# Kernel tuning notes

Measured on AMD Instinct MI355X. Metric: run time of the kernel, lower is better.

## Reference

```python
import jax, jax.numpy as jnp
import numpy as np

B, H, S, D = 2, 12, 2048, 64

def setup_inputs() -> dict:
    key = jax.random.key(0)
    kq, kk, kv = jax.random.split(key, 3)
    q = jax.random.normal(kq, (B, H, S, D), dtype=jnp.float32)
    k = jax.random.normal(kk, (B, H, S, D), dtype=jnp.float32)
    v = jax.random.normal(kv, (B, H, S, D), dtype=jnp.float32)
    attn_mask = jnp.zeros((1, 1, S, S), dtype=jnp.float32)
    return {"q": q, "k": k, "v": v, "attn_mask": attn_mask}

def reference(q, k, v, attn_mask):
    # scores: [B, H, S, S]
    scale = 1.0 / jnp.sqrt(jnp.asarray(q.shape[-1], q.dtype))
    attn = jnp.einsum('bhqd,bhkd->bhqk', q, k) * scale
    attn = attn + attn_mask  # additive mask, broadcast over batch/heads
    attn = jax.nn.softmax(attn, axis=-1)
    # dropout_ratio == 0.0 -> dropout is identity
    out = jnp.einsum('bhqk,bhkd->bhqd', attn, v)
    return out
```

## Files before the change

kernel.cpp:

```cpp
#include <hip/hip_runtime.h>
#include <hip/hip_bf16.h>
#include <stdint.h>

#define SLEN  2048
#define DHEAD 64
#define LOG2E 1.4426950408889634f
#define QSCALE (0.125f * LOG2E)

typedef short bf16x8 __attribute__((ext_vector_type(8)));
typedef float f32x4  __attribute__((ext_vector_type(4)));
typedef float f32x16 __attribute__((ext_vector_type(16)));
typedef unsigned short u16x8 __attribute__((ext_vector_type(8)));
typedef unsigned u32x2 __attribute__((ext_vector_type(2)));

static __device__ __forceinline__ unsigned short f2bf(float f) {
    union { float f; unsigned int u; } x; x.f = f;
    return (unsigned short)((x.u + 0x7FFFu + ((x.u >> 16) & 1u)) >> 16);
}

static __device__ __forceinline__ unsigned pk2(float lo, float hi) {
    __hip_bfloat162 h = __float22bfloat162_rn(make_float2(lo, hi));
    union { __hip_bfloat162 b; unsigned u; } c; c.b = h; return c.u;
}

static __device__ __forceinline__ u32x2 pl32(unsigned a, unsigned b) {
    return __builtin_amdgcn_permlane32_swap(a, b, false, false);
}
static __device__ __forceinline__ float    asf(unsigned u) { union { unsigned u; float f; } c; c.u = u; return c.f; }
static __device__ __forceinline__ unsigned asu(float f)    { union { float f; unsigned u; } c; c.f = f; return c.u; }
static __device__ __forceinline__ float max3(float a, float b, float c) {
    return fmaxf(fmaxf(a, b), c);
}

static __device__ __forceinline__ void gl_lds16(const void* g, void* l) {
    __builtin_amdgcn_global_load_lds(
        (const __attribute__((address_space(1))) unsigned int*)g,
        (__attribute__((address_space(3))) unsigned int*)l, 16, 0, 0);
}

__global__ __launch_bounds__(256)
void prep(const float* __restrict__ K, const float* __restrict__ V,
          const float* __restrict__ Mk, unsigned* __restrict__ flag, int maskN4,
          unsigned short* __restrict__ Kb, unsigned short* __restrict__ Vt)
{
    __shared__ unsigned short T[64][72];
    const int tid = threadIdx.x;
    const int st = blockIdx.x, bh = blockIdx.y;
    const size_t base = ((size_t)bh * SLEN + (size_t)st * 64) * DHEAD;

    #pragma unroll
    for (int it = 0; it < 4; ++it) {
        const int idx = it * 1024 + tid * 4;
        const int s = idx >> 6, d = idx & 63;
        float4 k4 = *(const float4*)(K + base + idx);
        float4 v4 = *(const float4*)(V + base + idx);
        ushort4 ko;
        ko.x = f2bf(k4.x); ko.y = f2bf(k4.y);
        ko.z = f2bf(k4.z); ko.w = f2bf(k4.w);
        *(ushort4*)(Kb + base + idx) = ko;
        T[d + 0][s] = f2bf(v4.x);
        T[d + 1][s] = f2bf(v4.y);
        T[d + 2][s] = f2bf(v4.z);
        T[d + 3][s] = f2bf(v4.w);
    }
    __syncthreads();
    const int d = tid >> 2, sc = (tid & 3) * 16;
    unsigned short* orow = Vt + ((size_t)bh * DHEAD + d) * SLEN + (size_t)st * 64 + sc;
    *(u16x8*)(orow)     = *(const u16x8*)&T[d][sc];
    *(u16x8*)(orow + 8) = *(const u16x8*)&T[d][sc + 8];

    const int nb  = gridDim.x * gridDim.y;
    const int bid = blockIdx.y * gridDim.x + blockIdx.x;
    unsigned any = 0;
    for (int i = bid * 256 + tid; i < maskN4; i += nb * 256) {
        float4 mv = *(const float4*)(Mk + (size_t)i * 4);
        any |= asu(mv.x) | asu(mv.y) | asu(mv.z) | asu(mv.w);
    }
    if (any) atomicOr(flag, 1u);
}

__global__ __launch_bounds__(256, 3)
void sdpa_fwd11(const float* __restrict__ Q,
                const unsigned short* __restrict__ Kb,
                const unsigned short* __restrict__ VtG,
                const float* __restrict__ M, const unsigned* __restrict__ flag,
                float* __restrict__ O,
                float* __restrict__ Opart, float* __restrict__ ML,
                int nsShift, int BH)
{
    __shared__ unsigned short Kt[2][64][64];
    __shared__ unsigned short Vt[2][64][64];

    const int tid  = threadIdx.x;
    const int wave = tid >> 6, lane = tid & 63;
    const int l31  = lane & 31, hi = lane >> 5;
    const bool hasMask = (*flag != 0);

    const int nwg  = gridDim.x;
    int wg = blockIdx.x;
    if ((nwg & 7) == 0) wg = (wg & 7) * (nwg >> 3) + (wg >> 3);
    const int qt    = wg & 15;
    const int rest  = wg >> 4;
    const int slice = rest & ((1 << nsShift) - 1);
    const int bh    = rest >> nsShift;

    const int kv0 = slice * (SLEN >> nsShift);
    const int NT  = (SLEN >> nsShift) >> 6;
    const int qrow = qt * 128 + wave * 32 + l31;
    const size_t hoff = (size_t)bh * SLEN * DHEAD;

    bf16x8 qf[4];
    {
        const float* qp = Q + hoff + (size_t)qrow * DHEAD + hi * 8;
        #pragma unroll
        for (int ds = 0; ds < 4; ++ds) {
            float4 a = *(const float4*)(qp + ds * 16);
            float4 b = *(const float4*)(qp + ds * 16 + 4);
            union { unsigned u[4]; bf16x8 v; } fq;
            fq.u[0] = pk2(a.x * QSCALE, a.y * QSCALE);
            fq.u[1] = pk2(a.z * QSCALE, a.w * QSCALE);
            fq.u[2] = pk2(b.x * QSCALE, b.y * QSCALE);
            fq.u[3] = pk2(b.z * QSCALE, b.w * QSCALE);
            qf[ds] = fq.v;
        }
    }

    const char* kgb = (const char*)(Kb + hoff) + (size_t)kv0 * 128;
    const char* vgb = (const char*)(VtG + (size_t)bh * DHEAD * SLEN) + (size_t)kv0 * 2;
    unsigned koff[2], voff[2], ldst[2];
    #pragma unroll
    for (int i = 0; i < 2; ++i) {
        const unsigned o = i * 4096 + tid * 16;
        const unsigned row = o >> 7;
        const unsigned slot = ((o >> 4) & 7) ^ (row & 7) ^ ((row >> 3) & 7);
        koff[i] = row * 128 + slot * 16;
        voff[i] = row * 4096 + slot * 16;
        ldst[i] = i * 4096 + wave * 1024;
    }

    f32x16 oacc[2];
    #pragma unroll
    for (int db = 0; db < 2; ++db)
        #pragma unroll
        for (int r = 0; r < 16; ++r) oacc[db][r] = 0.f;
    float m_i = -INFINITY, l_i = 0.f;

    auto STAGE = [&](int tt) {
        const unsigned bo = (unsigned)(tt & 1) * 8192;
        #pragma unroll
        for (int i = 0; i < 2; ++i) {
            gl_lds16(kgb + (size_t)tt * 8192 + koff[i], (char*)Kt + bo + ldst[i]);
            gl_lds16(vgb + (size_t)tt * 128  + voff[i], (char*)Vt + bo + ldst[i]);
        }
    };

    STAGE(0);

    for (int kt = 0; kt < NT; ++kt) {
        const int b0 = kt & 1;

        asm volatile("s_waitcnt vmcnt(0)" ::: "memory");
        __builtin_amdgcn_s_barrier();
        __builtin_amdgcn_sched_barrier(0);

        if (kt + 1 < NT) STAGE(kt + 1);

        float4 mq[8];
        if (hasMask) {
            const float* mrow = M + (size_t)qrow * SLEN + kv0 + kt * 64;
            #pragma unroll
            for (int sb = 0; sb < 2; ++sb)
                #pragma unroll
                for (int g = 0; g < 4; ++g)
                    mq[sb * 4 + g] = *(const float4*)(mrow + sb * 32 + g * 8 + hi * 4);
        }

        f32x16 sc[2];
        const char* kl = (const char*)Kt + b0 * 8192;
        __builtin_amdgcn_s_setprio(1);
        #pragma unroll
        for (int sb = 0; sb < 2; ++sb) {
            f32x16 acc;
            #pragma unroll
            for (int r = 0; r < 16; ++r) acc[r] = 0.f;
            const int row = sb * 32 + l31;
            const int rx = (row & 7) ^ ((row >> 3) & 7);
            #pragma unroll
            for (int ds = 0; ds < 4; ++ds) {
                const int slot = (ds * 2 + hi) ^ rx;
                bf16x8 kf = *(const bf16x8*)(kl + row * 128 + slot * 16);
                acc = __builtin_amdgcn_mfma_f32_32x32x16_bf16(kf, qf[ds], acc, 0, 0, 0);
            }
            sc[sb] = acc;
        }
        __builtin_amdgcn_s_setprio(0);

        if (hasMask) {
            #pragma unroll
            for (int sb = 0; sb < 2; ++sb)
                #pragma unroll
                for (int r = 0; r < 16; ++r)
                    sc[sb][r] = fmaf(mq[sb * 4 + (r >> 2)][r & 3], LOG2E, sc[sb][r]);
        }

        float red[8];
        #pragma unroll
        for (int r = 0; r < 8; ++r)
            red[r] = fmaxf(fmaxf(sc[0][r], sc[0][r + 8]),
                           fmaxf(sc[1][r], sc[1][r + 8]));
        float r0 = max3(red[0], red[1], red[2]);
        float r1 = max3(red[3], red[4], red[5]);
        float r2 = max3(fmaxf(red[6], red[7]), r0, r1);
        u32x2 pm = pl32(asu(r2), asu(r2));
        const float mtile = fmaxf(asf(pm.x), asf(pm.y));

        if (!__all(mtile - m_i <= 11.0f)) {
            const float mnew = fmaxf(m_i, mtile);
            const float alpha = __builtin_amdgcn_exp2f(m_i - mnew);
            l_i *= alpha;
            #pragma unroll
            for (int db = 0; db < 2; ++db)
                #pragma unroll
                for (int r = 0; r < 16; ++r) oacc[db][r] *= alpha;
            m_i = mnew;
        }

        #pragma unroll
        for (int sb = 0; sb < 2; ++sb)
            #pragma unroll
            for (int r = 0; r < 16; ++r)
                sc[sb][r] = __builtin_amdgcn_exp2f(sc[sb][r] - m_i);

        float sr[16];
        #pragma unroll
        for (int r = 0; r < 16; ++r) sr[r] = sc[0][r] + sc[1][r];
        #pragma unroll
        for (int r = 0; r < 8; ++r) sr[r] += sr[r + 8];
        #pragma unroll
        for (int r = 0; r < 4; ++r) sr[r] += sr[r + 4];
        sr[0] = (sr[0] + sr[2]) + (sr[1] + sr[3]);
        u32x2 ps = pl32(asu(sr[0]), asu(sr[0]));
        l_i += asf(ps.x) + asf(ps.y);

        unsigned wa[8], wb[8];
        #pragma unroll
        for (int sb = 0; sb < 2; ++sb)
            #pragma unroll
            for (int g = 0; g < 4; ++g) {
                wa[sb * 4 + g] = pk2(sc[sb][4 * g + 0], sc[sb][4 * g + 1]);
                wb[sb * 4 + g] = pk2(sc[sb][4 * g + 2], sc[sb][4 * g + 3]);
            }
        bf16x8 pf[4];
        #pragma unroll
        for (int ks = 0; ks < 4; ++ks) {
            u32x2 pa = pl32(wa[2 * ks], wa[2 * ks + 1]);
            u32x2 pb = pl32(wb[2 * ks], wb[2 * ks + 1]);
            union { unsigned u[4]; bf16x8 v; } f;
            f.u[0] = pa.x;
            f.u[1] = pb.x;
            f.u[2] = pa.y;
            f.u[3] = pb.y;
            pf[ks] = f.v;
        }

        const char* vl = (const char*)Vt + b0 * 8192;
        __builtin_amdgcn_s_setprio(1);
        #pragma unroll
        for (int db = 0; db < 2; ++db) {
            const int row = db * 32 + l31;
            const int rx = (row & 7) ^ ((row >> 3) & 7);
            #pragma unroll
            for (int ks = 0; ks < 4; ++ks) {
                const int slot = (ks * 2 + hi) ^ rx;
                bf16x8 vf = *(const bf16x8*)(vl + row * 128 + slot * 16);
                oacc[db] = __builtin_amdgcn_mfma_f32_32x32x16_bf16(vf, pf[ks], oacc[db], 0, 0, 0);
            }
        }
        __builtin_amdgcn_s_setprio(0);
    }

    if (nsShift == 0) {
        const float inv = 1.0f / l_i;
        float* op = O + hoff + (size_t)qrow * DHEAD;
        #pragma unroll
        for (int db = 0; db < 2; ++db)
            #pragma unroll
            for (int g = 0; g < 4; ++g) {
                float4 o4;
                o4.x = oacc[db][4 * g + 0] * inv;
                o4.y = oacc[db][4 * g + 1] * inv;
                o4.z = oacc[db][4 * g + 2] * inv;
                o4.w = oacc[db][4 * g + 3] * inv;
                *(float4*)(op + db * 32 + g * 8 + hi * 4) = o4;
            }
    } else {
        const size_t pidx = ((size_t)slice * BH + bh) * SLEN + qrow;
        float* op = Opart + pidx * DHEAD;
        #pragma unroll
        for (int db = 0; db < 2; ++db)
            #pragma unroll
            for (int g = 0; g < 4; ++g) {
                float4 o4;
                o4.x = oacc[db][4 * g + 0];
                o4.y = oacc[db][4 * g + 1];
                o4.z = oacc[db][4 * g + 2];
                o4.w = oacc[db][4 * g + 3];
                *(float4*)(op + db * 32 + g * 8 + hi * 4) = o4;
            }
        if (hi == 0) {
            ML[pidx * 2]     = m_i;
            ML[pidx * 2 + 1] = l_i;
        }
    }
}

__global__ __launch_bounds__(256)
void merge_partials(const float* __restrict__ Opart, const float* __restrict__ ML,
                    float* __restrict__ O, int NS, int BHS)
{
    const int gid = blockIdx.x * 256 + threadIdx.x;
    const int row = gid >> 4;
    const int c = (gid & 15) << 2;
    if (row >= BHS) return;

    float m = -INFINITY;
    for (int s = 0; s < NS; ++s)
        m = fmaxf(m, ML[((size_t)s * BHS + row) * 2]);

    float lsum = 0.f;
    float4 acc = make_float4(0.f, 0.f, 0.f, 0.f);
    for (int s = 0; s < NS; ++s) {
        const size_t pr = (size_t)s * BHS + row;
        const float w = __builtin_amdgcn_exp2f(ML[pr * 2] - m);
        lsum += w * ML[pr * 2 + 1];
        float4 v = *(const float4*)(Opart + pr * DHEAD + c);
        acc.x += w * v.x; acc.y += w * v.y;
        acc.z += w * v.z; acc.w += w * v.w;
    }
    const float inv = 1.0f / lsum;
    float4 o4;
    o4.x = acc.x * inv; o4.y = acc.y * inv;
    o4.z = acc.z * inv; o4.w = acc.w * inv;
    *(float4*)(O + (size_t)row * DHEAD + c) = o4;
}

__global__ __launch_bounds__(256)
void sdpa_fwd(const float* __restrict__ Q, const float* __restrict__ K,
              const float* __restrict__ V, const float* __restrict__ M,
              float* __restrict__ O)
{
    __shared__ unsigned short Klds[64][72];
    __shared__ unsigned short Vtl[64][72];
    __shared__ unsigned short Plds[4][16][72];

    const int tid  = threadIdx.x;
    const int wave = tid >> 6, lane = tid & 63;
    const int lg   = lane >> 4, ln = lane & 15;
    const int qtile = blockIdx.x, bh = blockIdx.y;
    const int qbase = qtile * 64 + wave * 16;
    const size_t hoff = (size_t)bh * SLEN * DHEAD;

    bf16x8 qf[2];
    {
        const float* qp = Q + hoff + (size_t)(qbase + ln) * DHEAD;
        #pragma unroll
        for (int ks = 0; ks < 2; ++ks) {
            float4 a = *(const float4*)(qp + ks * 32 + lg * 8);
            float4 b = *(const float4*)(qp + ks * 32 + lg * 8 + 4);
            qf[ks][0] = (short)f2bf(a.x * 0.125f); qf[ks][1] = (short)f2bf(a.y * 0.125f);
            qf[ks][2] = (short)f2bf(a.z * 0.125f); qf[ks][3] = (short)f2bf(a.w * 0.125f);
            qf[ks][4] = (short)f2bf(b.x * 0.125f); qf[ks][5] = (short)f2bf(b.y * 0.125f);
            qf[ks][6] = (short)f2bf(b.z * 0.125f); qf[ks][7] = (short)f2bf(b.w * 0.125f);
        }
    }

    f32x4 oacc[4];
    #pragma unroll
    for (int dn = 0; dn < 4; ++dn) oacc[dn] = (f32x4){0.f, 0.f, 0.f, 0.f};
    float m_i[4] = {-INFINITY, -INFINITY, -INFINITY, -INFINITY};
    float l_i[4] = {0.f, 0.f, 0.f, 0.f};

    for (int kt = 0; kt < SLEN / 64; ++kt) {
        const int kbase = kt * 64;
        __syncthreads();
        {
            const float* kp = K + hoff + (size_t)kbase * DHEAD;
            const float* vp = V + hoff + (size_t)kbase * DHEAD;
            #pragma unroll
            for (int it = 0; it < 4; ++it) {
                int flat = it * 1024 + tid * 4;
                int r = flat >> 6, c = flat & 63;
                float4 kv4 = *(const float4*)(kp + flat);
                float4 vv4 = *(const float4*)(vp + flat);
                ushort4 kb;
                kb.x = f2bf(kv4.x); kb.y = f2bf(kv4.y);
                kb.z = f2bf(kv4.z); kb.w = f2bf(kv4.w);
                *(ushort4*)&Klds[r][c] = kb;
                Vtl[c + 0][r] = f2bf(vv4.x); Vtl[c + 1][r] = f2bf(vv4.y);
                Vtl[c + 2][r] = f2bf(vv4.z); Vtl[c + 3][r] = f2bf(vv4.w);
            }
        }
        __syncthreads();

        f32x4 sc[4];
        #pragma unroll
        for (int nt = 0; nt < 4; ++nt) {
            f32x4 acc = (f32x4){0.f, 0.f, 0.f, 0.f};
            #pragma unroll
            for (int ks = 0; ks < 2; ++ks) {
                bf16x8 kf = *(const bf16x8*)&Klds[nt * 16 + ln][ks * 32 + lg * 8];
                acc = __builtin_amdgcn_mfma_f32_16x16x32_bf16(qf[ks], kf, acc, 0, 0, 0);
            }
            sc[nt] = acc;
        }
        #pragma unroll
        for (int i = 0; i < 4; ++i) {
            const float* mrow = M + (size_t)(qbase + 4 * lg + i) * SLEN + kbase;
            #pragma unroll
            for (int nt = 0; nt < 4; ++nt) sc[nt][i] += mrow[nt * 16 + ln];
        }
        float mnew[4], alpha[4];
        #pragma unroll
        for (int i = 0; i < 4; ++i) {
            float tm = fmaxf(fmaxf(sc[0][i], sc[1][i]), fmaxf(sc[2][i], sc[3][i]));
            tm = fmaxf(tm, __shfl_xor(tm, 1));
            tm = fmaxf(tm, __shfl_xor(tm, 2));
            tm = fmaxf(tm, __shfl_xor(tm, 4));
            tm = fmaxf(tm, __shfl_xor(tm, 8));
            mnew[i] = fmaxf(m_i[i], tm);
            alpha[i] = __expf(m_i[i] - mnew[i]);
            m_i[i] = mnew[i];
        }
        #pragma unroll
        for (int nt = 0; nt < 4; ++nt)
            #pragma unroll
            for (int i = 0; i < 4; ++i) {
                float p = __expf(sc[nt][i] - mnew[i]);
                sc[nt][i] = p;
                Plds[wave][4 * lg + i][nt * 16 + ln] = f2bf(p);
            }
        #pragma unroll
        for (int i = 0; i < 4; ++i) {
            float ts = (sc[0][i] + sc[1][i]) + (sc[2][i] + sc[3][i]);
            ts += __shfl_xor(ts, 1);
            ts += __shfl_xor(ts, 2);
            ts += __shfl_xor(ts, 4);
            ts += __shfl_xor(ts, 8);
            l_i[i] = l_i[i] * alpha[i] + ts;
            #pragma unroll
            for (int dn = 0; dn < 4; ++dn) oacc[dn][i] *= alpha[i];
        }
        #pragma unroll
        for (int ks = 0; ks < 2; ++ks) {
            bf16x8 pa = *(const bf16x8*)&Plds[wave][ln][ks * 32 + lg * 8];
            #pragma unroll
            for (int dn = 0; dn < 4; ++dn) {
                bf16x8 vb = *(const bf16x8*)&Vtl[dn * 16 + ln][ks * 32 + lg * 8];
                oacc[dn] = __builtin_amdgcn_mfma_f32_16x16x32_bf16(pa, vb, oacc[dn], 0, 0, 0);
            }
        }
    }
    #pragma unroll
    for (int i = 0; i < 4; ++i) {
        float inv = 1.0f / l_i[i];
        float* op = O + hoff + (size_t)(qbase + 4 * lg + i) * DHEAD;
        #pragma unroll
        for (int dn = 0; dn < 4; ++dn) op[dn * 16 + ln] = oacc[dn][i] * inv;
    }
}

extern "C" void kernel_launch(void* const* d_in, const int* in_sizes, int n_in,
                              void* d_out, int out_size, void* d_ws, size_t ws_size,
                              hipStream_t stream) {
    const float* q = (const float*)d_in[0];
    const float* k = (const float*)d_in[1];
    const float* v = (const float*)d_in[2];
    const float* m = (const float*)d_in[3];
    float* o = (float*)d_out;

    const int bh = in_sizes[0] / (SLEN * DHEAD);
    const int maskN = in_sizes[3];
    const size_t H = (size_t)bh * SLEN * DHEAD;
    const size_t BHS = (size_t)bh * SLEN;
    const size_t baseB = 2 * H * sizeof(unsigned short);

    if (ws_size < 16 + baseB) {
        sdpa_fwd<<<dim3(SLEN / 64, bh), 256, 0, stream>>>(q, k, v, m, o);
        return;
    }

    const size_t perS = H * sizeof(float) + BHS * 2 * sizeof(float);
    int nsShift = 0;
    if (ws_size >= 16 + baseB + 4 * perS)      nsShift = 2;
    else if (ws_size >= 16 + baseB + 2 * perS) nsShift = 1;
    const int NS = 1 << nsShift;

    unsigned* flag = (unsigned*)d_ws;
    unsigned short* kb = (unsigned short*)((char*)d_ws + 16);
    unsigned short* vt = kb + H;
    float* opart = (float*)((char*)d_ws + 16 + baseB);
    float* ml    = opart + (size_t)NS * H;

    hipMemsetAsync(flag, 0, 4, stream);
    prep<<<dim3(SLEN / 64, bh), 256, 0, stream>>>(k, v, m, flag, maskN / 4, kb, vt);
    sdpa_fwd11<<<16 * bh * NS, 256, 0, stream>>>(q, kb, vt, m, flag, o, opart, ml, nsShift, bh);
    if (NS > 1) {
        const int mb = (int)((BHS * 16 + 255) / 256);
        merge_partials<<<mb, 256, 0, stream>>>(opart, ml, o, NS, (int)BHS);
    }
}
```

Baseline: 80.96 us.

## Triple-buffer K/V staging, interleave P packing with PV MFMAs, cap KV split at two

K/V shared-memory staging goes from two buffers to three. The next tile's loads are now issued before the wait and barrier, and the wait only requires the current tile's loads to finish (vmcnt(4)), so the prefetch overlaps the barrier. The bf16 packing of P is split into halves and interleaved with the PV MFMAs to shorten register live ranges and overlap conversion with matrix work. The KV split is capped at two slices instead of up to four, which halves the grid and the partial-merge traffic but reduces parallelism. Shared memory per block grows to 48KB, which may press on the 3-blocks-per-CU occupancy target.

Measured after the change: 71.46 us. 1.13x faster.

```diff
diff --git a/kernel.cpp b/kernel.cpp
--- a/kernel.cpp
+++ b/kernel.cpp
@@ -80,7 +80,7 @@
 }
 
 __global__ __launch_bounds__(256, 3)
-void sdpa_fwd11(const float* __restrict__ Q,
+void sdpa_fwd12(const float* __restrict__ Q,
                 const unsigned short* __restrict__ Kb,
                 const unsigned short* __restrict__ VtG,
                 const float* __restrict__ M, const unsigned* __restrict__ flag,
@@ -88,8 +88,8 @@
                 float* __restrict__ Opart, float* __restrict__ ML,
                 int nsShift, int BH)
 {
-    __shared__ unsigned short Kt[2][64][64];
-    __shared__ unsigned short Vt[2][64][64];
+    __shared__ unsigned short Kt[3][64][64];
+    __shared__ unsigned short Vt[3][64][64];
 
     const int tid  = threadIdx.x;
     const int wave = tid >> 6, lane = tid & 63;
@@ -146,7 +146,7 @@
     float m_i = -INFINITY, l_i = 0.f;
 
     auto STAGE = [&](int tt) {
-        const unsigned bo = (unsigned)(tt & 1) * 8192;
+        const unsigned bo = (unsigned)(tt % 3) * 8192;
         #pragma unroll
         for (int i = 0; i < 2; ++i) {
             gl_lds16(kgb + (size_t)tt * 8192 + koff[i], (char*)Kt + bo + ldst[i]);
@@ -157,13 +157,16 @@
     STAGE(0);
 
     for (int kt = 0; kt < NT; ++kt) {
-        const int b0 = kt & 1;
-
-        asm volatile("s_waitcnt vmcnt(0)" ::: "memory");
+        const int b0 = kt % 3;
+
+        if (kt + 1 < NT) {
+            STAGE(kt + 1);
+            asm volatile("s_waitcnt vmcnt(4)" ::: "memory");
+        } else {
+            asm volatile("s_waitcnt vmcnt(0)" ::: "memory");
+        }
         __builtin_amdgcn_s_barrier();
         __builtin_amdgcn_sched_barrier(0);
-
-        if (kt + 1 < NT) STAGE(kt + 1);
 
         float4 mq[8];
         if (hasMask) {
@@ -242,38 +245,39 @@
         u32x2 ps = pl32(asu(sr[0]), asu(sr[0]));
         l_i += asf(ps.x) + asf(ps.y);
 
-        unsigned wa[8], wb[8];
-        #pragma unroll
-        for (int sb = 0; sb < 2; ++sb)
-            #pragma unroll
-            for (int g = 0; g < 4; ++g) {
-                wa[sb * 4 + g] = pk2(sc[sb][4 * g + 0], sc[sb][4 * g + 1]);
-                wb[sb * 4 + g] = pk2(sc[sb][4 * g + 2], sc[sb][4 * g + 3]);
-            }
-        bf16x8 pf[4];
-        #pragma unroll
-        for (int ks = 0; ks < 4; ++ks) {
-            u32x2 pa = pl32(wa[2 * ks], wa[2 * ks + 1]);
-            u32x2 pb = pl32(wb[2 * ks], wb[2 * ks + 1]);
-            union { unsigned u[4]; bf16x8 v; } f;
-            f.u[0] = pa.x;
-            f.u[1] = pb.x;
-            f.u[2] = pa.y;
-            f.u[3] = pb.y;
-            pf[ks] = f.v;
-        }
-
         const char* vl = (const char*)Vt + b0 * 8192;
         __builtin_amdgcn_s_setprio(1);
         #pragma unroll
-        for (int db = 0; db < 2; ++db) {
-            const int row = db * 32 + l31;
-            const int rx = (row & 7) ^ ((row >> 3) & 7);
-            #pragma unroll
-            for (int ks = 0; ks < 4; ++ks) {
-                const int slot = (ks * 2 + hi) ^ rx;
-                bf16x8 vf = *(const bf16x8*)(vl + row * 128 + slot * 16);
-                oacc[db] = __builtin_amdgcn_mfma_f32_32x32x16_bf16(vf, pf[ks], oacc[db], 0, 0, 0);
+        for (int half = 0; half < 2; ++half) {
+            bf16x8 pf[2];
+            #pragma unroll
+            for (int kk = 0; kk < 2; ++kk) {
+                const int g0 = half * 2 + kk;
+                unsigned wa0 = pk2(sc[half][8 * kk + 0], sc[half][8 * kk + 1]);
+                unsigned wb0 = pk2(sc[half][8 * kk + 2], sc[half][8 * kk + 3]);
+                unsigned wa1 = pk2(sc[half][8 * kk + 4], sc[half][8 * kk + 5]);
+                unsigned wb1 = pk2(sc[half][8 * kk + 6], sc[half][8 * kk + 7]);
+                u32x2 pa = pl32(wa0, wa1);
+                u32x2 pb = pl32(wb0, wb1);
+                union { unsigned u[4]; bf16x8 v; } f;
+                f.u[0] = pa.x;
+                f.u[1] = pb.x;
+                f.u[2] = pa.y;
+                f.u[3] = pb.y;
+                pf[kk] = f.v;
+                (void)g0;
+            }
+            #pragma unroll
+            for (int db = 0; db < 2; ++db) {
+                const int row = db * 32 + l31;
+                const int rx = (row & 7) ^ ((row >> 3) & 7);
+                #pragma unroll
+                for (int kk = 0; kk < 2; ++kk) {
+                    const int ks = half * 2 + kk;
+                    const int slot = (ks * 2 + hi) ^ rx;
+                    bf16x8 vf = *(const bf16x8*)(vl + row * 128 + slot * 16);
+                    oacc[db] = __builtin_amdgcn_mfma_f32_32x32x16_bf16(vf, pf[kk], oacc[db], 0, 0, 0);
+                }
             }
         }
         __builtin_amdgcn_s_setprio(0);
@@ -490,9 +494,7 @@
     }
 
     const size_t perS = H * sizeof(float) + BHS * 2 * sizeof(float);
-    int nsShift = 0;
-    if (ws_size >= 16 + baseB + 4 * perS)      nsShift = 2;
-    else if (ws_size >= 16 + baseB + 2 * perS) nsShift = 1;
+    int nsShift = (ws_size >= 16 + baseB + 2 * perS) ? 1 : 0;
     const int NS = 1 << nsShift;
 
     unsigned* flag = (unsigned*)d_ws;
@@ -503,7 +505,7 @@
 
     hipMemsetAsync(flag, 0, 4, stream);
     prep<<<dim3(SLEN / 64, bh), 256, 0, stream>>>(k, v, m, flag, maskN / 4, kb, vt);
-    sdpa_fwd11<<<16 * bh * NS, 256, 0, stream>>>(q, kb, vt, m, flag, o, opart, ml, nsShift, bh);
+    sdpa_fwd12<<<16 * bh * NS, 256, 0, stream>>>(q, kb, vt, m, flag, o, opart, ml, nsShift, bh);
     if (NS > 1) {
         const int mb = (int)((BHS * 16 + 255) / 256);
         merge_partials<<<mb, 256, 0, stream>>>(opart, ml, o, NS, (int)BHS);
```
